# Kernel tuning notes

Measured on AMD Instinct MI355X. Metric: run time of the kernel, lower is better.

The kernel has to match this reference:

```python
import jax, jax.numpy as jnp
import numpy as np

N, E, G = 50000, 200000, 512
F_N, F_E, H, L = 64, 16, 32, 3
EPS = 1e-5


def setup_inputs() -> dict:
    key = jax.random.key(0)
    ks = jax.random.split(key, 20)
    s = 0.1
    inp = {
        'x': jax.random.normal(ks[0], (N, F_N), jnp.float32),
        'edge_attr': jax.random.normal(ks[1], (E, F_E), jnp.float32),
        'W_node': jax.random.normal(ks[2], (F_N, H), jnp.float32) * s,
        'b_node': jnp.zeros((H,), jnp.float32),
        'W_edge': jax.random.normal(ks[3], (F_E, 2 * F_E), jnp.float32) * s,
        'b_edge': jnp.zeros((2 * F_E,), jnp.float32),
        'W_nn': jax.random.normal(ks[4], (L, 2 * F_E, H * H), jnp.float32) * s,
        'b_nn': jnp.zeros((L, H * H), jnp.float32),
        'W_root': jax.random.normal(ks[5], (L, H, H), jnp.float32) * s,
        'b_conv': jnp.zeros((L, H), jnp.float32),
        'gamma': jnp.ones((L, H), jnp.float32),
        'beta': jnp.zeros((L, H), jnp.float32),
        'W2': jax.random.normal(ks[6], (H, H // 2), jnp.float32) * s,
        'b2': jnp.zeros((H // 2,), jnp.float32),
        'W3': jax.random.normal(ks[7], (H // 2, 1), jnp.float32) * s,
        'b3': jnp.zeros((1,), jnp.float32),
        'edge_index': jax.random.randint(ks[8], (2, E), 0, N, jnp.int32),
        'batch': jnp.sort(jax.random.randint(ks[9], (N,), 0, G, jnp.int32)),
    }
    return inp


def reference(x, edge_attr, W_node, b_node, W_edge, b_edge, W_nn, b_nn,
              W_root, b_conv, gamma, beta, W2, b2, W3, b3, edge_index, batch):
    src, dst = edge_index[0], edge_index[1]
    h = x @ W_node + b_node                      # [N,H] node_emb
    ea = edge_attr @ W_edge + b_edge             # [E,2*F_E] edge_emb
    for l in range(L):
        # NNConv: per-edge weight matrix from edge features
        We = (ea @ W_nn[l] + b_nn[l]).reshape(E, H, H)   # [E,H,H]
        m = jnp.einsum('ei,eio->eo', h[src], We)         # gather + per-edge transform
        agg = jax.ops.segment_sum(m, dst, num_segments=N)  # scatter-add aggregation
        h = h @ W_root[l] + agg + b_conv[l]
        # BatchNorm (batch statistics over nodes) + ReLU
        mu = h.mean(axis=0)
        var = h.var(axis=0)
        h = jax.nn.relu((h - mu) * jax.lax.rsqrt(var + EPS) * gamma[l] + beta[l])
    # global mean pool over graphs
    cnt = jax.ops.segment_sum(jnp.ones((N,), h.dtype), batch, num_segments=G)
    gsum = jax.ops.segment_sum(h, batch, num_segments=G)
    gx = gsum / jnp.maximum(cnt, 1.0)[:, None]   # [G,H]
    # head: lin2 -> relu -> (dropout=identity at eval) -> lin3
    hh = jax.nn.relu(gx @ W2 + b2)
    return hh @ W3 + b3                          # [G,1]
```

## Files before the change

kernel.cpp:

```cpp
#include <hip/hip_runtime.h>

#define NN 50000
#define NE 200000
#define NG 512
#define NBK 16
#define NB 3125
#define FN 64
#define FE 16
#define H 32
#define NL 3
#define EPSV 1e-5f

__global__ void k_prep(const float* __restrict__ Wnn, const float* __restrict__ We,
                       const float* __restrict__ be, const float* __restrict__ Bnn,
                       float* __restrict__ V2, float* __restrict__ M,
                       const int* __restrict__ src, const int* __restrict__ batch,
                       int* __restrict__ degB, float* __restrict__ cnt,
                       const float* __restrict__ x, const float* __restrict__ Wn,
                       const float* __restrict__ bno, float* __restrict__ h,
                       float* __restrict__ agg) {
    __shared__ float smem[2048];
    int t = threadIdx.x;
    int b = blockIdx.x;
    if (b < 96) {
        int l = b >> 5, i = b & 31;
        float* sWnn = smem;
        float* sWe  = smem + 1024;
        for (int j = t; j < 1024; j += 256)
            sWnn[j] = Wnn[((size_t)(l * 32 + (j >> 5))) * 1024 + i * 32 + (j & 31)];
        for (int j = t; j < 512; j += 256) sWe[j] = We[j];
        __syncthreads();
#pragma unroll
        for (int cc = 0; cc < 2; cc++) {
            int c = 2 * t + cc;
            int f = c >> 5, o = c & 31;
            float v = 0.f;
#pragma unroll
            for (int k = 0; k < 32; k++) v += sWe[f * 32 + k] * sWnn[k * 32 + o];
            V2[(size_t)(l * 32 + i) * 512 + c] = v;
        }
        if (t < 32) {
            float m = Bnn[(size_t)l * 1024 + i * 32 + t];
            for (int k = 0; k < 32; k++) m += be[k] * sWnn[k * 32 + t];
            M[l * 1024 + i * 32 + t] = m;
        }
    } else if (b < 878) {
        for (int j = t; j < FN * H; j += 256) smem[j] = Wn[j];
        __syncthreads();
        int n0 = (b - 96) * 64;
        int node8 = t >> 5, o = t & 31;
        for (int r = 0; r < 8; r++) {
            int n = n0 + r * 8 + node8;
            if (n < NN) {
                const float* xr = x + (size_t)n * FN;
                float acc = bno[o];
#pragma unroll 16
                for (int i = 0; i < FN; i++) acc += xr[i] * smem[i * H + o];
                size_t idx = (size_t)n * H + o;
                h[idx] = acc;
                agg[idx] = 0.f;
            }
        }
    } else {
        int e = (b - 878) * 256 + t;
        if (e < NE) atomicAdd(&degB[src[e] >> 4], 1);
        if (e < NN) atomicAdd(&cnt[batch[e]], 1.f);
    }
}

__global__ void k_scanB(const int* __restrict__ degB, int* __restrict__ rowptrB,
                        int* __restrict__ cursorB) {
    __shared__ int ssum[1024];
    int t = threadIdx.x;
    int loc[4];
    int base = t * 4;
    int s = 0;
#pragma unroll
    for (int i = 0; i < 4; i++) {
        int idx = base + i;
        loc[i] = (idx < NB) ? degB[idx] : 0;
        s += loc[i];
    }
    ssum[t] = s;
    for (int off = 1; off < 1024; off <<= 1) {
        __syncthreads();
        int tv = (t >= off) ? ssum[t - off] : 0;
        __syncthreads();
        ssum[t] += tv;
    }
    __syncthreads();
    int run = ssum[t] - s;
#pragma unroll
    for (int i = 0; i < 4; i++) {
        int idx = base + i;
        if (idx < NB) { rowptrB[idx] = run; cursorB[idx] = run; run += loc[i]; }
    }
    if (t == 1023) rowptrB[NB] = ssum[1023];
}

__global__ void k_fill(const int* __restrict__ src, const int* __restrict__ dst,
                       const float* __restrict__ eattr, int* __restrict__ cursorB,
                       unsigned* __restrict__ sdR, float* __restrict__ eaR) {
    int e = blockIdx.x * 256 + threadIdx.x;
    if (e >= NE) return;
    int s = src[e];
    int p = atomicAdd(&cursorB[s >> 4], 1);
    sdR[p] = ((unsigned)dst[e] << 4) | (unsigned)(s & 15);
    const float4* q = (const float4*)(eattr + (size_t)e * FE);
    float4* r = (float4*)(eaR + (size_t)p * FE);
    float4 q0 = q[0], q1 = q[1], q2 = q[2], q3 = q[3];
    r[0] = q0; r[1] = q1; r[2] = q2; r[3] = q3;
}

__global__ __launch_bounds__(256, 4) void k_conv(
    const float* __restrict__ h0, const unsigned* __restrict__ sdR,
    const float* __restrict__ eaR,
    const float* __restrict__ V2l, const float* __restrict__ Ml,
    const int* __restrict__ rowptrB,
    float* __restrict__ agg, float* __restrict__ z,
    const float* __restrict__ statsPrev, float* __restrict__ statsZero,
    const float* __restrict__ gm, const float* __restrict__ bt,
    const float* __restrict__ Wr, const float* __restrict__ bc, int first) {
    __shared__ __align__(16) float sU[NBK][512];
    __shared__ __align__(16) float shh[NBK][32];
    __shared__ __align__(16) float su[NBK][32];
    int t = threadIdx.x;
    int nb0 = blockIdx.x * NBK;
    if (blockIdx.x == 0 && t < 64) statsZero[t] = 0.f;

#pragma unroll
    for (int r = 0; r < 2; r++) {
        int node = (t >> 5) + r * 8;
        int o = t & 31;
        size_t idx = (size_t)(nb0 + node) * H + o;
        float hv;
        if (first) {
            hv = h0[idx];
        } else {
            const float invn = 1.0f / (float)NN;
            float mu = statsPrev[o] * invn;
            float var = statsPrev[32 + o] * invn - mu * mu;
            float v = (z[idx] - mu) * rsqrtf(var + EPSV) * gm[o] + bt[o];
            hv = v > 0.f ? v : 0.f;
        }
        shh[node][o] = hv;
        __builtin_amdgcn_wave_barrier();
        float a = bc[o], bacc = 0.f;
#pragma unroll
        for (int i = 0; i < H; i++) {
            float hh = shh[node][i];
            a += hh * Wr[i * H + o];
            bacc += hh * Ml[i * H + o];
        }
        z[idx] = a;
        su[node][o] = bacc;
    }
    __syncthreads();

    {
        const float* vp = V2l + 2 * t;
        float2 acc[NBK];
#pragma unroll
        for (int n = 0; n < NBK; n++) acc[n] = make_float2(0.f, 0.f);
#pragma unroll
        for (int i4 = 0; i4 < 8; i4++) {
            float2 v0 = *(const float2*)(vp + (size_t)(i4 * 4 + 0) * 512);
            float2 v1 = *(const float2*)(vp + (size_t)(i4 * 4 + 1) * 512);
            float2 v2 = *(const float2*)(vp + (size_t)(i4 * 4 + 2) * 512);
            float2 v3 = *(const float2*)(vp + (size_t)(i4 * 4 + 3) * 512);
#pragma unroll
            for (int n = 0; n < NBK; n++) {
                float4 hv = *(const float4*)&shh[n][i4 * 4];
                acc[n].x += hv.x * v0.x + hv.y * v1.x + hv.z * v2.x + hv.w * v3.x;
                acc[n].y += hv.x * v0.y + hv.y * v1.y + hv.z * v2.y + hv.w * v3.y;
            }
        }
#pragma unroll
        for (int n = 0; n < NBK; n++)
            *(float2*)&sU[n][2 * t] = acc[n];
    }
    __syncthreads();

    int E0 = rowptrB[blockIdx.x], E1 = rowptrB[blockIdx.x + 1];
    int w = t >> 6;
    int lane = t & 63;
    int hw = lane >> 5;
    int o = lane & 31;
    for (int jb = E0 + 4 * w; jb < E1; jb += 16) {
        int ja = jb + 2 * hw;
        bool a0 = (ja < E1);
        bool a1 = (ja + 1 < E1);
        unsigned sd0 = 0, sd1 = 0;
        float4 e00 = make_float4(0.f, 0.f, 0.f, 0.f), e01 = e00, e02 = e00, e03 = e00;
        float4 e10 = e00, e11 = e00, e12 = e00, e13 = e00;
        if (a0) {
            sd0 = sdR[ja];
            const float4* p0 = (const float4*)(eaR + (size_t)ja * FE);
            e00 = p0[0]; e01 = p0[1]; e02 = p0[2]; e03 = p0[3];
        }
        if (a1) {
            sd1 = sdR[ja + 1];
            const float4* p1 = (const float4*)(eaR + (size_t)(ja + 1) * FE);
            e10 = p1[0]; e11 = p1[1]; e12 = p1[2]; e13 = p1[3];
        }
        if (a0) {
            int sn = sd0 & 15;
            unsigned d = sd0 >> 4;
            const float* tp = &sU[sn][0];
            float m = su[sn][o];
            m += e00.x * tp[0 * 32 + o] + e00.y * tp[1 * 32 + o]
               + e00.z * tp[2 * 32 + o] + e00.w * tp[3 * 32 + o];
            m += e01.x * tp[4 * 32 + o] + e01.y * tp[5 * 32 + o]
               + e01.z * tp[6 * 32 + o] + e01.w * tp[7 * 32 + o];
            m += e02.x * tp[8 * 32 + o] + e02.y * tp[9 * 32 + o]
               + e02.z * tp[10 * 32 + o] + e02.w * tp[11 * 32 + o];
            m += e03.x * tp[12 * 32 + o] + e03.y * tp[13 * 32 + o]
               + e03.z * tp[14 * 32 + o] + e03.w * tp[15 * 32 + o];
            atomicAdd(&agg[(size_t)d * H + o], m);
        }
        if (a1) {
            int sn = sd1 & 15;
            unsigned d = sd1 >> 4;
            const float* tp = &sU[sn][0];
            float m = su[sn][o];
            m += e10.x * tp[0 * 32 + o] + e10.y * tp[1 * 32 + o]
               + e10.z * tp[2 * 32 + o] + e10.w * tp[3 * 32 + o];
            m += e11.x * tp[4 * 32 + o] + e11.y * tp[5 * 32 + o]
               + e11.z * tp[6 * 32 + o] + e11.w * tp[7 * 32 + o];
            m += e12.x * tp[8 * 32 + o] + e12.y * tp[9 * 32 + o]
               + e12.z * tp[10 * 32 + o] + e12.w * tp[11 * 32 + o];
            m += e13.x * tp[12 * 32 + o] + e13.y * tp[13 * 32 + o]
               + e13.z * tp[14 * 32 + o] + e13.w * tp[15 * 32 + o];
            atomicAdd(&agg[(size_t)d * H + o], m);
        }
    }
}

__global__ void k_add_stats(float* __restrict__ z, float* __restrict__ agg,
                            float* __restrict__ stats) {
    __shared__ float red[256];
    int t = threadIdx.x;
    float s = 0.f, s2 = 0.f;
    for (size_t idx = (size_t)blockIdx.x * 256 + t; idx < (size_t)NN * H;
         idx += (size_t)gridDim.x * 256) {
        float v = z[idx] + agg[idx];
        z[idx] = v;
        agg[idx] = 0.f;
        s += v;
        s2 += v * v;
    }
    red[t] = s;
    __syncthreads();
    for (int st = 128; st >= 32; st >>= 1) {
        if (t < st) red[t] += red[t + st];
        __syncthreads();
    }
    if (t < 32) atomicAdd(&stats[t], red[t]);
    __syncthreads();
    red[t] = s2;
    __syncthreads();
    for (int st = 128; st >= 32; st >>= 1) {
        if (t < st) red[t] += red[t + st];
        __syncthreads();
    }
    if (t < 32) atomicAdd(&stats[32 + t], red[t]);
}

__global__ void k_bn_pool(const float* __restrict__ z, const float* __restrict__ stats,
                          const float* __restrict__ gm, const float* __restrict__ bt,
                          const int* __restrict__ batch, float* __restrict__ gsum) {
    int idx = blockIdx.x * 256 + threadIdx.x;
    if (idx >= NN * H) return;
    int n = idx >> 5, o = idx & 31;
    const float invn = 1.0f / (float)NN;
    float mu = stats[o] * invn;
    float var = stats[32 + o] * invn - mu * mu;
    float v = (z[idx] - mu) * rsqrtf(var + EPSV) * gm[o] + bt[o];
    v = v > 0.f ? v : 0.f;
    atomicAdd(&gsum[(size_t)batch[n] * H + o], v);
}

__global__ void k_head(const float* __restrict__ gsum, const float* __restrict__ cnt,
                       const float* __restrict__ W2, const float* __restrict__ b2,
                       const float* __restrict__ W3, const float* __restrict__ b3,
                       float* __restrict__ out) {
    __shared__ float sW2[H * 16];
    __shared__ float sW3[16];
    __shared__ float sb2[16];
    int t = threadIdx.x;
    for (int j = t; j < H * 16; j += 256) sW2[j] = W2[j];
    if (t < 16) { sW3[t] = W3[t]; sb2[t] = b2[t]; }
    __syncthreads();
    int g = blockIdx.x * 256 + t;
    if (g >= NG) return;
    float inv = 1.0f / fmaxf(cnt[g], 1.0f);
    float gx[H];
#pragma unroll
    for (int i = 0; i < H; i++) gx[i] = gsum[g * H + i] * inv;
    float o3 = b3[0];
#pragma unroll
    for (int j = 0; j < 16; j++) {
        float hh = sb2[j];
#pragma unroll
        for (int i = 0; i < H; i++) hh += gx[i] * sW2[i * 16 + j];
        hh = hh > 0.f ? hh : 0.f;
        o3 += hh * sW3[j];
    }
    out[g] = o3;
}

extern "C" void kernel_launch(void* const* d_in, const int* in_sizes, int n_in,
                              void* d_out, int out_size, void* d_ws, size_t ws_size,
                              hipStream_t stream) {
    const float* x      = (const float*)d_in[0];
    const float* eattr  = (const float*)d_in[1];
    const float* W_node = (const float*)d_in[2];
    const float* b_node = (const float*)d_in[3];
    const float* W_edge = (const float*)d_in[4];
    const float* b_edge = (const float*)d_in[5];
    const float* W_nn   = (const float*)d_in[6];
    const float* b_nn   = (const float*)d_in[7];
    const float* W_root = (const float*)d_in[8];
    const float* b_conv = (const float*)d_in[9];
    const float* gamma  = (const float*)d_in[10];
    const float* beta   = (const float*)d_in[11];
    const float* W2     = (const float*)d_in[12];
    const float* b2     = (const float*)d_in[13];
    const float* W3     = (const float*)d_in[14];
    const float* b3     = (const float*)d_in[15];
    const int* eidx     = (const int*)d_in[16];
    const int* batch    = (const int*)d_in[17];
    const int* src = eidx;
    const int* dst = eidx + NE;
    float* out = (float*)d_out;

    const size_t NNH = (size_t)NN * H;
    float* ws = (float*)d_ws;
    float* h      = ws;
    float* z      = h + NNH;
    float* agg    = z + NNH;
    float* stats  = agg + NNH;
    float* V2     = stats + 128;
    float* M      = V2 + (size_t)NL * 32 * 512;
    int*   degB   = (int*)(M + NL * 1024);
    float* gsum   = (float*)(degB + NB);
    float* cnt    = gsum + (size_t)NG * H;
    int*   rowptrB = (int*)(cnt + NG);
    int*   cursorB = rowptrB + NB + 1;
    unsigned* sdR = (unsigned*)(cursorB + NB);
    float* eaR    = (float*)(sdR + NE);

    hipMemsetAsync(degB, 0, (NB + NG * H + NG) * sizeof(int), stream);

    k_prep<<<96 + 782 + 782, 256, 0, stream>>>(
        W_nn, W_edge, b_edge, b_nn, V2, M, src, batch, degB, cnt,
        x, W_node, b_node, h, agg);
    k_scanB<<<1, 1024, 0, stream>>>(degB, rowptrB, cursorB);
    k_fill<<<(NE + 255) / 256, 256, 0, stream>>>(src, dst, eattr, cursorB, sdR, eaR);

    for (int l = 0; l < NL; l++) {
        float* statsCur  = stats + (l & 1) * 64;
        float* statsPrev = stats + ((l + 1) & 1) * 64;
        int lp = (l > 0) ? (l - 1) : 0;
        k_conv<<<NB, 256, 0, stream>>>(h, sdR, eaR, V2 + (size_t)l * 32 * 512,
                                       M + (size_t)l * 1024,
                                       rowptrB, agg, z,
                                       statsPrev, statsCur,
                                       gamma + lp * H, beta + lp * H,
                                       W_root + (size_t)l * H * H, b_conv + l * H,
                                       l == 0 ? 1 : 0);
        k_add_stats<<<512, 256, 0, stream>>>(z, agg, statsCur);
    }

    k_bn_pool<<<(NN * H + 255) / 256, 256, 0, stream>>>(
        z, stats + ((NL - 1) & 1) * 64,
        gamma + (NL - 1) * H, beta + (NL - 1) * H, batch, gsum);
    k_head<<<2, 256, 0, stream>>>(gsum, cnt, W2, b2, W3, b3, out);
}
```

Before: 377.3 us.

## Stage x tile in LDS, privatize graph counts, vectorize add_stats with float4

The node-embedding blocks of the prep kernel now load their 64-row x tile into shared memory with float4 loads instead of having each thread re-read x rows from global memory. Graph node counts move to new dedicated blocks that accumulate into shared-memory bins before issuing global atomics, which avoids heavy contention on 512 addresses. The add-stats kernel switches to float4 loads and stores with float4 shared reductions and a doubled grid. Together these target memory bandwidth and atomic contention in small kernels, at the cost of more LDS per block in the prep kernel.

Result: slower. 603.4 us (+59.9%).

```diff
diff --git a/kernel.cpp b/kernel.cpp
--- a/kernel.cpp
+++ b/kernel.cpp
@@ -19,7 +19,7 @@
                        const float* __restrict__ x, const float* __restrict__ Wn,
                        const float* __restrict__ bno, float* __restrict__ h,
                        float* __restrict__ agg) {
-    __shared__ float smem[2048];
+    __shared__ __align__(16) float smem[6144];
     int t = threadIdx.x;
     int b = blockIdx.x;
     if (b < 96) {
@@ -45,26 +45,45 @@
             M[l * 1024 + i * 32 + t] = m;
         }
     } else if (b < 878) {
-        for (int j = t; j < FN * H; j += 256) smem[j] = Wn[j];
-        __syncthreads();
+        float* sW = smem;
+        float* sx = smem + 2048;
+        for (int j = t; j < FN * H; j += 256) sW[j] = Wn[j];
         int n0 = (b - 96) * 64;
+        for (int j = t; j < 1024; j += 256) {
+            int row = j >> 4, c4 = j & 15;
+            if (n0 + row < NN)
+                *(float4*)&sx[row * FN + c4 * 4] =
+                    *(const float4*)(x + (size_t)(n0 + row) * FN + c4 * 4);
+        }
+        __syncthreads();
         int node8 = t >> 5, o = t & 31;
         for (int r = 0; r < 8; r++) {
-            int n = n0 + r * 8 + node8;
+            int node = r * 8 + node8;
+            int n = n0 + node;
             if (n < NN) {
-                const float* xr = x + (size_t)n * FN;
+                const float* xr = &sx[node * FN];
                 float acc = bno[o];
 #pragma unroll 16
-                for (int i = 0; i < FN; i++) acc += xr[i] * smem[i * H + o];
+                for (int i = 0; i < FN; i++) acc += xr[i] * sW[i * H + o];
                 size_t idx = (size_t)n * H + o;
                 h[idx] = acc;
                 agg[idx] = 0.f;
             }
         }
-    } else {
+    } else if (b < 1660) {
         int e = (b - 878) * 256 + t;
         if (e < NE) atomicAdd(&degB[src[e] >> 4], 1);
-        if (e < NN) atomicAdd(&cnt[batch[e]], 1.f);
+    } else {
+        float* bins = smem;
+        for (int j = t; j < NG; j += 256) bins[j] = 0.f;
+        __syncthreads();
+        int n = (b - 1660) * 256 + t;
+        if (n < NN) atomicAdd(&bins[batch[n]], 1.f);
+        __syncthreads();
+        for (int j = t; j < NG; j += 256) {
+            float v = bins[j];
+            if (v != 0.f) atomicAdd(&cnt[j], v);
+        }
     }
 }
 
@@ -238,32 +257,56 @@
 
 __global__ void k_add_stats(float* __restrict__ z, float* __restrict__ agg,
                             float* __restrict__ stats) {
-    __shared__ float red[256];
+    __shared__ __align__(16) float4 red[256];
     int t = threadIdx.x;
-    float s = 0.f, s2 = 0.f;
-    for (size_t idx = (size_t)blockIdx.x * 256 + t; idx < (size_t)NN * H;
-         idx += (size_t)gridDim.x * 256) {
-        float v = z[idx] + agg[idx];
-        z[idx] = v;
-        agg[idx] = 0.f;
-        s += v;
-        s2 += v * v;
+    float4 s = make_float4(0.f, 0.f, 0.f, 0.f), s2 = s;
+    const float4 zero = make_float4(0.f, 0.f, 0.f, 0.f);
+    float4* z4 = (float4*)z;
+    float4* a4 = (float4*)agg;
+    const size_t N4 = (size_t)NN * H / 4;
+    for (size_t i = (size_t)blockIdx.x * 256 + t; i < N4; i += (size_t)gridDim.x * 256) {
+        float4 zv = z4[i], av = a4[i];
+        float4 v = make_float4(zv.x + av.x, zv.y + av.y, zv.z + av.z, zv.w + av.w);
+        z4[i] = v;
+        a4[i] = zero;
+        s.x += v.x; s.y += v.y; s.z += v.z; s.w += v.w;
+        s2.x += v.x * v.x; s2.y += v.y * v.y; s2.z += v.z * v.z; s2.w += v.w * v.w;
     }
     red[t] = s;
     __syncthreads();
-    for (int st = 128; st >= 32; st >>= 1) {
-        if (t < st) red[t] += red[t + st];
-        __syncthreads();
-    }
-    if (t < 32) atomicAdd(&stats[t], red[t]);
+    for (int st = 128; st >= 8; st >>= 1) {
+        if (t < st) {
+            float4 o = red[t + st];
+            float4 m = red[t];
+            red[t] = make_float4(m.x + o.x, m.y + o.y, m.z + o.z, m.w + o.w);
+        }
+        __syncthreads();
+    }
+    if (t < 8) {
+        float4 v = red[t];
+        atomicAdd(&stats[4 * t + 0], v.x);
+        atomicAdd(&stats[4 * t + 1], v.y);
+        atomicAdd(&stats[4 * t + 2], v.z);
+        atomicAdd(&stats[4 * t + 3], v.w);
+    }
     __syncthreads();
     red[t] = s2;
     __syncthreads();
-    for (int st = 128; st >= 32; st >>= 1) {
-        if (t < st) red[t] += red[t + st];
-        __syncthreads();
-    }
-    if (t < 32) atomicAdd(&stats[32 + t], red[t]);
+    for (int st = 128; st >= 8; st >>= 1) {
+        if (t < st) {
+            float4 o = red[t + st];
+            float4 m = red[t];
+            red[t] = make_float4(m.x + o.x, m.y + o.y, m.z + o.z, m.w + o.w);
+        }
+        __syncthreads();
+    }
+    if (t < 8) {
+        float4 v = red[t];
+        atomicAdd(&stats[32 + 4 * t + 0], v.x);
+        atomicAdd(&stats[32 + 4 * t + 1], v.y);
+        atomicAdd(&stats[32 + 4 * t + 2], v.z);
+        atomicAdd(&stats[32 + 4 * t + 3], v.w);
+    }
 }
 
 __global__ void k_bn_pool(const float* __restrict__ z, const float* __restrict__ stats,
@@ -352,7 +395,7 @@
 
     hipMemsetAsync(degB, 0, (NB + NG * H + NG) * sizeof(int), stream);
 
-    k_prep<<<96 + 782 + 782, 256, 0, stream>>>(
+    k_prep<<<96 + 782 + 782 + 196, 256, 0, stream>>>(
         W_nn, W_edge, b_edge, b_nn, V2, M, src, batch, degB, cnt,
         x, W_node, b_node, h, agg);
     k_scanB<<<1, 1024, 0, stream>>>(degB, rowptrB, cursorB);
@@ -369,7 +412,7 @@
                                        gamma + lp * H, beta + lp * H,
                                        W_root + (size_t)l * H * H, b_conv + l * H,
                                        l == 0 ? 1 : 0);
-        k_add_stats<<<512, 256, 0, stream>>>(z, agg, statsCur);
+        k_add_stats<<<1024, 256, 0, stream>>>(z, agg, statsCur);
     }
 
     k_bn_pool<<<(NN * H + 255) / 256, 256, 0, stream>>>(
```
